# Performance work log

Hardware: AMD Instinct MI355X
Metric: run time of the kernel (lower is better)

The kernel has to match this reference:

```python
import jax, jax.numpy as jnp
import numpy as np
import math

NUM_LAYERS = 2
NUM_HEADS = 8
D_MODEL = 256
D_FF = 4 * D_MODEL
FACTOR = 5
B, L, F_IN = 8, 2048, 32


def layer_norm(x, g, b, eps=1e-5):
    m = x.mean(-1, keepdims=True)
    v = ((x - m) ** 2).mean(-1, keepdims=True)
    return (x - m) * jax.lax.rsqrt(v + eps) * g + b


def prob_attention(q, k, v, idx):
    # q,k,v: [B,H,L,Dh]; idx: [L,S] sampled key indices per query (ProbSparse)
    Bq, H, Lq, Dh = q.shape
    u = min(FACTOR * math.ceil(math.log(Lq)), Lq)  # number of 'active' queries
    k_s = k[:, :, idx, :]                              # [B,H,L,S,Dh] gathered keys
    qk_s = jnp.einsum('bhld,bhlsd->bhls', q, k_s)      # sampled scores
    M = qk_s.max(-1) - qk_s.sum(-1) / Lq               # sparsity measure [B,H,L]
    _, top = jax.lax.top_k(M, u)                       # [B,H,u] active query idx
    q_red = jnp.take_along_axis(q, top[..., None], axis=2)   # [B,H,u,Dh]
    scores = jnp.einsum('bhud,bhld->bhul', q_red, k) * (1.0 / math.sqrt(Dh))
    attn = jax.nn.softmax(scores, axis=-1)             # [B,H,u,L]
    upd = jnp.einsum('bhul,bhld->bhud', attn, v)       # [B,H,u,Dh]
    # initial context = mean of V (mask_flag=False), then scatter active rows
    ctx = jnp.broadcast_to(v.mean(2, keepdims=True), (Bq, H, Lq, Dh))
    bi = jnp.arange(Bq)[:, None, None]
    hi = jnp.arange(H)[None, :, None]
    return ctx.at[bi, hi, top].set(upd)


def setup_inputs() -> dict:
    key = jax.random.key(0)
    ks = jax.random.split(key, 16)
    S = min(FACTOR * math.ceil(math.log(L)), L)  # 40
    std = 0.02

    def w(k, shape):
        return jax.random.normal(k, shape, jnp.float32) * std

    inp = {}
    inp['x'] = jax.random.normal(ks[0], (B, L, F_IN), jnp.float32)
    inp['idx_sample'] = jax.random.randint(ks[1], (NUM_LAYERS, L, S), 0, L)
    inp['w_in'] = w(ks[2], (F_IN, D_MODEL)); inp['b_in'] = jnp.zeros((D_MODEL,), jnp.float32)
    inp['wq'] = w(ks[3], (NUM_LAYERS, D_MODEL, D_MODEL)); inp['bq'] = jnp.zeros((NUM_LAYERS, D_MODEL), jnp.float32)
    inp['wk'] = w(ks[4], (NUM_LAYERS, D_MODEL, D_MODEL)); inp['bk'] = jnp.zeros((NUM_LAYERS, D_MODEL), jnp.float32)
    inp['wv'] = w(ks[5], (NUM_LAYERS, D_MODEL, D_MODEL)); inp['bv'] = jnp.zeros((NUM_LAYERS, D_MODEL), jnp.float32)
    inp['wo'] = w(ks[6], (NUM_LAYERS, D_MODEL, D_MODEL)); inp['bo'] = jnp.zeros((NUM_LAYERS, D_MODEL), jnp.float32)
    inp['w_ff1'] = w(ks[7], (NUM_LAYERS, D_MODEL, D_FF)); inp['b_ff1'] = jnp.zeros((NUM_LAYERS, D_FF), jnp.float32)
    inp['w_ff2'] = w(ks[8], (NUM_LAYERS, D_FF, D_MODEL)); inp['b_ff2'] = jnp.zeros((NUM_LAYERS, D_MODEL), jnp.float32)
    inp['ln1_g'] = jnp.ones((NUM_LAYERS, D_MODEL), jnp.float32); inp['ln1_b'] = jnp.zeros((NUM_LAYERS, D_MODEL), jnp.float32)
    inp['ln2_g'] = jnp.ones((NUM_LAYERS, D_MODEL), jnp.float32); inp['ln2_b'] = jnp.zeros((NUM_LAYERS, D_MODEL), jnp.float32)
    inp['w_fc1'] = w(ks[9], (D_MODEL, 64)); inp['b_fc1'] = jnp.zeros((64,), jnp.float32)
    inp['w_fc2'] = w(ks[10], (64, 1)); inp['b_fc2'] = jnp.zeros((1,), jnp.float32)
    return inp


def reference(x, idx_sample, w_in, b_in, wq, bq, wk, bk, wv, bv, wo, bo,
              w_ff1, b_ff1, w_ff2, b_ff2, ln1_g, ln1_b, ln2_g, ln2_b,
              w_fc1, b_fc1, w_fc2, b_fc2):
    Bx, Lx, _ = x.shape
    h = x @ w_in + b_in  # [B,L,D_MODEL]
    for i in range(NUM_LAYERS):
        q = (h @ wq[i] + bq[i]).reshape(Bx, Lx, NUM_HEADS, -1).transpose(0, 2, 1, 3)
        k = (h @ wk[i] + bk[i]).reshape(Bx, Lx, NUM_HEADS, -1).transpose(0, 2, 1, 3)
        v = (h @ wv[i] + bv[i]).reshape(Bx, Lx, NUM_HEADS, -1).transpose(0, 2, 1, 3)
        ctx = prob_attention(q, k, v, idx_sample[i])            # [B,H,L,Dh]
        ctx = ctx.transpose(0, 2, 1, 3).reshape(Bx, Lx, D_MODEL)
        new_x = ctx @ wo[i] + bo[i]
        h = layer_norm(h + new_x, ln1_g[i], ln1_b[i])
        y = jax.nn.relu(h @ w_ff1[i] + b_ff1[i]) @ w_ff2[i] + b_ff2[i]
        h = layer_norm(h + y, ln2_g[i], ln2_b[i])
    last = h[:, -1, :]                      # take final time step
    out = jax.nn.relu(last @ w_fc1 + b_fc1) @ w_fc2 + b_fc2
    return out[:, None, :]                  # unsqueeze(1) -> [B,1,output_size]
```

## Files before the change

### kernel.cpp

```cpp
#include <hip/hip_runtime.h>
#include <math.h>

#define BB 8
#define LL 2048
#define DM 256
#define NH 8
#define DH 32
#define DFF 1024
#define SS 40
#define UU 40
#define BL (BB*LL)
#define NSL 8

#define SCP 260
#define KP  40
#define VP  34

typedef unsigned short ushort_t;
typedef unsigned char uchar_t;
typedef __attribute__((ext_vector_type(8))) short short8;
typedef __attribute__((ext_vector_type(4))) float f32x4;

__device__ inline ushort_t f2b(float f)
{
    unsigned int u = __float_as_uint(f);
    u += 0x7fff + ((u >> 16) & 1);
    return (ushort_t)(u >> 16);
}

__device__ inline float blo(unsigned int u) { return __uint_as_float(u << 16); }
__device__ inline float bhi(unsigned int u) { return __uint_as_float(u & 0xffff0000u); }

__device__ inline void gload16(const void* g, const void* l)
{
    __builtin_amdgcn_global_load_lds(
        (const __attribute__((address_space(1))) unsigned int*)g,
        (__attribute__((address_space(3))) unsigned int*)l, 16, 0, 0);
}

template<int RELU, int OUT_MODE>
__global__ __launch_bounds__(256)
void gemm_mfma(const ushort_t* __restrict__ A, const ushort_t* __restrict__ Bt,
               const float* __restrict__ bias, void* __restrict__ Cout,
               void* __restrict__ aux, int M, int N, int K)
{
    __shared__ ushort_t Asl[128 * 32];
    __shared__ ushort_t Bsl[128 * 32];

    const int t    = threadIdx.x;
    const int lane = t & 63;
    const int wv   = t >> 6;
    const int row0 = blockIdx.x * 128;
    const int col0 = blockIdx.y * 128;
    const int wr   = (wv >> 1) * 64;
    const int wc   = (wv & 1) * 64;
    const int quad = lane >> 4;
    const int l16  = lane & 15;

    f32x4 acc[4][4];
    #pragma unroll
    for (int i = 0; i < 4; ++i)
        #pragma unroll
        for (int j = 0; j < 4; ++j)
            acc[i][j] = 0.f;

    for (int k0 = 0; k0 < K; k0 += 32) {
        __syncthreads();
        #pragma unroll
        for (int r = 0; r < 2; ++r) {
            int g = r * 256 + t;
            const ushort_t* ga = A  + (size_t)(row0 + (g >> 2)) * K + k0 + (g & 3) * 8;
            const ushort_t* gb = Bt + (size_t)(col0 + (g >> 2)) * K + k0 + (g & 3) * 8;
            int lbase = (r * 256 + wv * 64) * 16;
            gload16(ga, (const char*)Asl + lbase);
            gload16(gb, (const char*)Bsl + lbase);
        }
        __syncthreads();

        short8 af[4], bfr[4];
        #pragma unroll
        for (int mi = 0; mi < 4; ++mi)
            af[mi] = *(const short8*)&Asl[(wr + mi * 16 + l16) * 32 + quad * 8];
        #pragma unroll
        for (int ni = 0; ni < 4; ++ni)
            bfr[ni] = *(const short8*)&Bsl[(wc + ni * 16 + l16) * 32 + quad * 8];
        #pragma unroll
        for (int mi = 0; mi < 4; ++mi)
            #pragma unroll
            for (int ni = 0; ni < 4; ++ni)
                acc[mi][ni] = __builtin_amdgcn_mfma_f32_16x16x32_bf16(
                    af[mi], bfr[ni], acc[mi][ni], 0, 0, 0);
    }

    #pragma unroll
    for (int mi = 0; mi < 4; ++mi) {
        #pragma unroll
        for (int ni = 0; ni < 4; ++ni) {
            int col = col0 + wc + ni * 16 + l16;
            float bb = bias[col];
            #pragma unroll
            for (int r = 0; r < 4; ++r) {
                int row = row0 + wr + mi * 16 + quad * 4 + r;
                float v = acc[mi][ni][r] + bb;
                if (RELU) v = v > 0.f ? v : 0.f;
                if (OUT_MODE == 0) {
                    ((float*)Cout)[(size_t)row * N + col] = v;
                } else if (OUT_MODE == 1) {
                    int tensor = col >> 8;
                    int c2 = col & 255;
                    int b  = row >> 11, l = row & (LL - 1);
                    int hh = c2 >> 5,  dh = c2 & 31;
                    int bh = b * NH + hh;
                    size_t bi = (((size_t)bh * LL + l) << 5) + dh;
                    ushort_t vb16 = f2b(v);
                    ((ushort_t*)Cout)[(size_t)tensor * (BB*NH*LL*DH) + bi] = vb16;
                    if (tensor == 1)
                        ((ushort_t*)aux)[(((size_t)l << 6) + bh) * 32 + dh] = vb16;
                } else if (OUT_MODE == 2) {
                    ((ushort_t*)Cout)[(size_t)row * N + col] = f2b(v);
                } else {
                    ((float*)Cout)[(size_t)row * N + col] = v;
                    ((ushort_t*)aux)[(size_t)row * N + col] = f2b(v);
                }
            }
        }
    }
}

template<int HEAD>
__global__ __launch_bounds__(256)
void gemmln_k(const ushort_t* __restrict__ A, const ushort_t* __restrict__ Bt,
              const float* __restrict__ bias, float* __restrict__ h,
              ushort_t* __restrict__ hb, const float* __restrict__ g,
              const float* __restrict__ beta, int K,
              const float* __restrict__ w1, const float* __restrict__ b1,
              const float* __restrict__ w2, const float* __restrict__ b2,
              float* __restrict__ out)
{
    __shared__ ushort_t Asl[32 * 32];
    __shared__ ushort_t Bsl[256 * 32];
    __shared__ float rs[4][32], rs2[4][32];
    __shared__ float hrowS[256];

    const int t    = threadIdx.x;
    const int lane = t & 63;
    const int wv   = t >> 6;
    const int row0 = blockIdx.x * 32;
    const int wc   = wv * 64;
    const int quad = lane >> 4;
    const int l16  = lane & 15;

    f32x4 acc[2][4];
    #pragma unroll
    for (int i = 0; i < 2; ++i)
        #pragma unroll
        for (int j = 0; j < 4; ++j)
            acc[i][j] = 0.f;

    for (int k0 = 0; k0 < K; k0 += 32) {
        __syncthreads();
        if (wv < 2) {
            const ushort_t* ga = A + (size_t)(row0 + (t >> 2)) * K + k0 + (t & 3) * 8;
            gload16(ga, (const char*)Asl + wv * 1024);
        }
        #pragma unroll
        for (int r = 0; r < 4; ++r) {
            int gg = r * 256 + t;
            const ushort_t* gb = Bt + (size_t)(gg >> 2) * K + k0 + (gg & 3) * 8;
            gload16(gb, (const char*)Bsl + (r * 256 + wv * 64) * 16);
        }
        __syncthreads();

        short8 af[2], bfr[4];
        #pragma unroll
        for (int mi = 0; mi < 2; ++mi)
            af[mi] = *(const short8*)&Asl[(mi * 16 + l16) * 32 + quad * 8];
        #pragma unroll
        for (int ni = 0; ni < 4; ++ni)
            bfr[ni] = *(const short8*)&Bsl[(wc + ni * 16 + l16) * 32 + quad * 8];
        #pragma unroll
        for (int mi = 0; mi < 2; ++mi)
            #pragma unroll
            for (int ni = 0; ni < 4; ++ni)
                acc[mi][ni] = __builtin_amdgcn_mfma_f32_16x16x32_bf16(
                    af[mi], bfr[ni], acc[mi][ni], 0, 0, 0);
    }

    float gcol[4], bcol[4];
    #pragma unroll
    for (int ni = 0; ni < 4; ++ni) {
        int col = wc + ni * 16 + l16;
        gcol[ni] = g[col];
        bcol[ni] = beta[col];
    }
    float ps[2][4], ps2[2][4];
    #pragma unroll
    for (int mi = 0; mi < 2; ++mi) {
        #pragma unroll
        for (int r = 0; r < 4; ++r) {
            int row = row0 + mi * 16 + quad * 4 + r;
            float s = 0.f, s2 = 0.f;
            #pragma unroll
            for (int ni = 0; ni < 4; ++ni) {
                int col = wc + ni * 16 + l16;
                float v = acc[mi][ni][r] + bias[col] + h[(size_t)row * DM + col];
                acc[mi][ni][r] = v;
                s += v;
                s2 += v * v;
            }
            ps[mi][r] = s;
            ps2[mi][r] = s2;
        }
    }
    #pragma unroll
    for (int off = 1; off < 16; off <<= 1) {
        #pragma unroll
        for (int mi = 0; mi < 2; ++mi)
            #pragma unroll
            for (int r = 0; r < 4; ++r) {
                ps[mi][r]  += __shfl_xor(ps[mi][r],  off, 16);
                ps2[mi][r] += __shfl_xor(ps2[mi][r], off, 16);
            }
    }
    if (l16 == 0) {
        #pragma unroll
        for (int mi = 0; mi < 2; ++mi)
            #pragma unroll
            for (int r = 0; r < 4; ++r) {
                int lrow = mi * 16 + quad * 4 + r;
                rs[wv][lrow]  = ps[mi][r];
                rs2[wv][lrow] = ps2[mi][r];
            }
    }
    __syncthreads();

    #pragma unroll
    for (int mi = 0; mi < 2; ++mi) {
        #pragma unroll
        for (int r = 0; r < 4; ++r) {
            int lrow = mi * 16 + quad * 4 + r;
            int row  = row0 + lrow;
            float tot  = rs[0][lrow] + rs[1][lrow] + rs[2][lrow] + rs[3][lrow];
            float tot2 = rs2[0][lrow] + rs2[1][lrow] + rs2[2][lrow] + rs2[3][lrow];
            float mean = tot * (1.f / (float)DM);
            float var  = tot2 * (1.f / (float)DM) - mean * mean;
            float inv  = 1.0f / sqrtf(var + 1e-5f);
            #pragma unroll
            for (int ni = 0; ni < 4; ++ni) {
                int col = wc + ni * 16 + l16;
                float val = (acc[mi][ni][r] - mean) * inv * gcol[ni] + bcol[ni];
                h[(size_t)row * DM + col]  = val;
                hb[(size_t)row * DM + col] = f2b(val);
                if (HEAD && lrow == 31) hrowS[col] = val;
            }
        }
    }

    if (HEAD) {
        __syncthreads();
        if ((blockIdx.x & 63) == 63 && t < 64) {
            int b = blockIdx.x >> 6;
            float s = 0.f;
            for (int kk = 0; kk < DM; ++kk)
                s = fmaf(hrowS[kk], w1[kk * 64 + t], s);
            s += b1[t];
            s = s > 0.f ? s : 0.f;
            float contrib = s * w2[t];
            #pragma unroll
            for (int off = 32; off > 0; off >>= 1)
                contrib += __shfl_down(contrib, off, 64);
            if (t == 0) out[b] = contrib + b2[0];
        }
    }
}

__device__ inline void tcvt_dev(float (*tile)[33], const float* __restrict__ src,
                                ushort_t* __restrict__ dst, int K, int N,
                                int matStride, int bi)
{
    int tilesN = N >> 5;
    int tpm = (K >> 5) * tilesN;
    int m   = bi / tpm;
    int tid = bi % tpm;
    int k0 = (tid / tilesN) << 5, n0 = (tid % tilesN) << 5;
    const float* s = src + (size_t)m * K * N;
    ushort_t*    d = dst + (size_t)m * matStride;
    int r = threadIdx.x >> 5, c = threadIdx.x & 31;
    #pragma unroll
    for (int i = 0; i < 4; ++i)
        tile[r + 8 * i][c] = s[(size_t)(k0 + r + 8 * i) * N + n0 + c];
    __syncthreads();
    #pragma unroll
    for (int i = 0; i < 4; ++i)
        d[(size_t)(n0 + r + 8 * i) * K + k0 + c] = f2b(tile[c][r + 8 * i]);
}

__global__ __launch_bounds__(256)
void preproc_k(const float* __restrict__ wq, const float* __restrict__ wk,
               const float* __restrict__ wv, const float* __restrict__ wo,
               const float* __restrict__ wf1, const float* __restrict__ wf2,
               const float* __restrict__ w_in,
               const float* __restrict__ bq, const float* __restrict__ bk,
               const float* __restrict__ bv, const float* __restrict__ x,
               ushort_t* __restrict__ wqkvT, ushort_t* __restrict__ woT,
               ushort_t* __restrict__ wf1T, ushort_t* __restrict__ wf2T,
               ushort_t* __restrict__ w_inT, float* __restrict__ bqkv,
               ushort_t* __restrict__ xb16)
{
    __shared__ float tile[32][33];
    int b = blockIdx.x;
    if (b < 512) {
        int which = b >> 7, lb = b & 127;
        const float* src = which == 0 ? wq : which == 1 ? wk : which == 2 ? wv : wo;
        ushort_t* dst = which == 0 ? wqkvT : which == 1 ? wqkvT + 65536
                       : which == 2 ? wqkvT + 131072 : woT;
        int stride = which == 3 ? 65536 : 768 * 256;
        tcvt_dev(tile, src, dst, DM, DM, stride, lb);
    } else if (b < 1024) {
        tcvt_dev(tile, wf1, wf1T, DM, DFF, 1024 * 256, b - 512);
    } else if (b < 1536) {
        tcvt_dev(tile, wf2, wf2T, DFF, DM, 256 * 1024, b - 1024);
    } else if (b < 1544) {
        tcvt_dev(tile, w_in, w_inT, 32, DM, 256 * 32, b - 1536);
    } else if (b < 1550) {
        int t = (b - 1544) * 256 + threadIdx.x;
        int i = t / 768, j = t % 768;
        const float* s = j < 256 ? bq : (j < 512 ? bk : bv);
        bqkv[t] = s[i * 256 + (j & 255)];
    } else {
        int tid = (b - 1550) * 256 + threadIdx.x;
        float4 v = ((const float4*)x)[tid];
        unsigned int lo = f2b(v.x) | ((unsigned int)f2b(v.y) << 16);
        unsigned int hi = f2b(v.z) | ((unsigned int)f2b(v.w) << 16);
        ((uint2*)xb16)[tid] = make_uint2(lo, hi);
    }
}

__global__ __launch_bounds__(256)
void metric2_k(const ushort_t* __restrict__ qb16, const ushort_t* __restrict__ kT,
               const int* __restrict__ idx, float* __restrict__ Mout,
               unsigned int* __restrict__ jidx32)
{
    __shared__ float mst[64][5];
    int t = threadIdx.x;
    int w = t >> 6, lane = t & 63;
    int l = blockIdx.x * 4 + w;

    if (t < 64) {
        int zb = t >> 3, sel = t & 7;
        int zl = blockIdx.x * 4 + (sel >> 1), half = sel & 1;
        jidx32[(size_t)(zb * LL + zl) * 2 + half] = 0;
    }

    float4 q[8];
    {
        const uint4* qr4 = (const uint4*)(qb16 + ((size_t)(lane * LL + l) << 5));
        #pragma unroll
        for (int i = 0; i < 4; ++i) {
            uint4 u = qr4[i];
            q[2 * i]     = make_float4(blo(u.x), bhi(u.x), blo(u.y), bhi(u.y));
            q[2 * i + 1] = make_float4(blo(u.z), bhi(u.z), blo(u.w), bhi(u.w));
        }
    }

    int r40 = idx[l * SS + (lane < SS ? lane : SS - 1)];

    float mx = -3e38f, sm = 0.f;
    for (int s = 0; s < SS; ++s) {
        int r = __shfl(r40, s, 64);
        const uint4* kr = (const uint4*)(kT + (((size_t)r << 6) + lane) * 32);
        float d = 0.f;
        #pragma unroll
        for (int ww = 0; ww < 4; ++ww) {
            uint4 kv = kr[ww];
            float4 qa = q[2 * ww], qb2 = q[2 * ww + 1];
            d = fmaf(blo(kv.x), qa.x, d);
            d = fmaf(bhi(kv.x), qa.y, d);
            d = fmaf(blo(kv.y), qa.z, d);
            d = fmaf(bhi(kv.y), qa.w, d);
            d = fmaf(blo(kv.z), qb2.x, d);
            d = fmaf(bhi(kv.z), qb2.y, d);
            d = fmaf(blo(kv.w), qb2.z, d);
            d = fmaf(bhi(kv.w), qb2.w, d);
        }
        mx = fmaxf(mx, d);
        sm += d;
    }
    mst[lane][w] = mx - sm * (1.0f / (float)LL);
    __syncthreads();

    int bh = t >> 2, ls = t & 3;
    Mout[(size_t)bh * LL + blockIdx.x * 4 + ls] = mst[bh][ls];
}

__global__ __launch_bounds__(512)
void topkf_k(const float* __restrict__ Mout, int* __restrict__ top,
             uchar_t* __restrict__ jidx)
{
    __shared__ float cvS[320];
    __shared__ int   ciS[320];
    int bh = blockIdx.x;
    int t  = threadIdx.x;
    int lane = t & 63, w = t >> 6;
    int l0 = w << 8;

    float v[4];
    #pragma unroll
    for (int i = 0; i < 4; ++i)
        v[i] = Mout[(size_t)bh * LL + l0 + i * 64 + lane];

    for (int r = 0; r < UU; ++r) {
        float bv = -3e38f; int bi = 1 << 30;
        #pragma unroll
        for (int i = 0; i < 4; ++i) {
            int idx = l0 + i * 64 + lane;
            if (v[i] > bv || (v[i] == bv && idx < bi)) { bv = v[i]; bi = idx; }
        }
        #pragma unroll
        for (int off = 32; off > 0; off >>= 1) {
            float ov = __shfl_down(bv, off, 64);
            int   oi = __shfl_down(bi, off, 64);
            if (ov > bv || (ov == bv && oi < bi)) { bv = ov; bi = oi; }
        }
        bv = __shfl(bv, 0, 64);
        bi = __shfl(bi, 0, 64);
        if (lane == 0) { cvS[w * UU + r] = bv; ciS[w * UU + r] = bi; }
        int rel = bi - l0;
        if ((rel & 63) == lane) v[rel >> 6] = -3e38f;
    }
    __syncthreads();

    for (int c = t; c < 320; c += 512) {
        float mv = cvS[c]; int mi = ciS[c];
        int rank = 0;
        for (int j = 0; j < 320; ++j)
            rank += (cvS[j] > mv) || (cvS[j] == mv && ciS[j] < mi);
        if (rank < UU) {
            top[bh * UU + rank] = mi;
            int b = bh >> 3, hh = bh & 7;
            jidx[(size_t)(b * LL + mi) * 8 + hh] = (uchar_t)(rank + 1);
        }
    }
}

__global__ __launch_bounds__(256)
void attnupd_k(const ushort_t* __restrict__ qb16, const ushort_t* __restrict__ kb16,
               const ushort_t* __restrict__ vb16, const int* __restrict__ top,
               float* __restrict__ mP, float* __restrict__ sP,
               float* __restrict__ OP, float* __restrict__ vmeanP)
{
    __shared__ ushort_t qs[48 * KP];
    __shared__ ushort_t kv[256 * KP];
    __shared__ float    sc[48 * SCP];
    __shared__ float    msh[UU];
    __shared__ float    red[8][32];

    int blk = blockIdx.x;
    int sl  = blk & (NSL - 1);
    int bh  = blk >> 3;
    int t   = threadIdx.x;
    int l0  = sl << 8;
    int lane = t & 63, wvx = t >> 6;
    int quad = lane >> 4, l16 = lane & 15;
    const float scale = 0.17677669529663687f;

    for (int i = t; i < 48 * 32; i += 256) {
        int j = i >> 5, dd = i & 31;
        qs[(i >> 5) * KP + dd] = (j < UU)
            ? qb16[((size_t)(bh * LL + top[bh * UU + j]) << 5) + dd] : (ushort_t)0;
    }
    {
        const unsigned int* krow =
            (const unsigned int*)(kb16 + ((size_t)(bh * LL + l0 + t) << 5));
        #pragma unroll
        for (int i = 0; i < 16; ++i)
            ((unsigned int*)kv)[t * (KP / 2) + i] = krow[i];
    }
    __syncthreads();

    {
        short8 afq[3];
        #pragma unroll
        for (int mt = 0; mt < 3; ++mt)
            afq[mt] = *(const short8*)&qs[(mt * 16 + l16) * KP + quad * 8];
        #pragma unroll
        for (int n4 = 0; n4 < 4; ++n4) {
            int nt = wvx * 4 + n4;
            short8 bk = *(const short8*)&kv[(nt * 16 + l16) * KP + quad * 8];
            #pragma unroll
            for (int mt = 0; mt < 3; ++mt) {
                f32x4 dd = {0.f, 0.f, 0.f, 0.f};
                dd = __builtin_amdgcn_mfma_f32_16x16x32_bf16(afq[mt], bk, dd, 0, 0, 0);
                #pragma unroll
                for (int r = 0; r < 4; ++r)
                    sc[(mt * 16 + quad * 4 + r) * SCP + nt * 16 + l16] = dd[r] * scale;
            }
        }
    }
    __syncthreads();

    int j8 = t >> 5, d = t & 31;
    #pragma unroll
    for (int g = 0; g < 5; ++g) {
        int j = g * 8 + j8;
        float4 a = *(const float4*)&sc[j * SCP + 4 * d];
        float4 b = *(const float4*)&sc[j * SCP + 128 + 4 * d];
        float m = fmaxf(fmaxf(fmaxf(a.x, a.y), fmaxf(a.z, a.w)),
                        fmaxf(fmaxf(b.x, b.y), fmaxf(b.z, b.w)));
        #pragma unroll
        for (int off = 16; off > 0; off >>= 1)
            m = fmaxf(m, __shfl_down(m, off, 64));
        if (d == 0) msh[j] = m;
    }
    __syncthreads();

    #pragma unroll 2
    for (int i = t; i < UU * 64; i += 256) {
        int j = i >> 6;
        float* p = &sc[j * SCP + (i & 63) * 4];
        float4 e = *(float4*)p;
        float mm = msh[j];
        e.x = __expf(e.x - mm); e.y = __expf(e.y - mm);
        e.z = __expf(e.z - mm); e.w = __expf(e.w - mm);
        *(float4*)p = e;
    }
    __syncthreads();

    int pq = bh * NSL + sl;

    #pragma unroll
    for (int g = 0; g < 5; ++g) {
        int j = g * 8 + j8;
        float4 a = *(const float4*)&sc[j * SCP + 4 * d];
        float4 b = *(const float4*)&sc[j * SCP + 128 + 4 * d];
        float s = a.x + a.y + a.z + a.w + b.x + b.y + b.z + b.w;
        #pragma unroll
        for (int off = 16; off > 0; off >>= 1)
            s += __shfl_down(s, off, 64);
        if (d == 0) { sP[pq * UU + j] = s; mP[pq * UU + j] = msh[j]; }
    }
    {
        const unsigned int* vrow =
            (const unsigned int*)(vb16 + ((size_t)(bh * LL + l0 + t) << 5));
        #pragma unroll
        for (int i = 0; i < 16; ++i)
            *(unsigned int*)&kv[t * VP + 2 * i] = vrow[i];
        const ushort_t* base = vb16 + ((size_t)(bh * LL + l0 + j8 * 32) << 5) + d;
        float s = 0.f;
        #pragma unroll 8
        for (int i = 0; i < 32; ++i)
            s += __uint_as_float((unsigned int)base[(size_t)i << 5] << 16);
        red[j8][d] = s;
    }
    __syncthreads();

    if (t < 32) {
        float tot = 0.f;
        #pragma unroll
        for (int p = 0; p < 8; ++p) tot += red[p][t];
        vmeanP[pq * 32 + t] = tot;
    }

    if (wvx < 3) {
        f32x4 acc0 = {0.f, 0.f, 0.f, 0.f};
        f32x4 acc1 = {0.f, 0.f, 0.f, 0.f};
        #pragma unroll
        for (int ks = 0; ks < 8; ++ks) {
            float4 p0 = *(const float4*)&sc[(wvx * 16 + l16) * SCP + ks * 32 + quad * 8];
            float4 p1 = *(const float4*)&sc[(wvx * 16 + l16) * SCP + ks * 32 + quad * 8 + 4];
            short8 af;
            af[0] = (short)f2b(p0.x); af[1] = (short)f2b(p0.y);
            af[2] = (short)f2b(p0.z); af[3] = (short)f2b(p0.w);
            af[4] = (short)f2b(p1.x); af[5] = (short)f2b(p1.y);
            af[6] = (short)f2b(p1.z); af[7] = (short)f2b(p1.w);
            #pragma unroll
            for (int nt = 0; nt < 2; ++nt) {
                short8 bf;
                #pragma unroll
                for (int jj = 0; jj < 8; ++jj)
                    bf[jj] = (short)kv[(ks * 32 + quad * 8 + jj) * VP + nt * 16 + l16];
                if (nt == 0)
                    acc0 = __builtin_amdgcn_mfma_f32_16x16x32_bf16(af, bf, acc0, 0, 0, 0);
                else
                    acc1 = __builtin_amdgcn_mfma_f32_16x16x32_bf16(af, bf, acc1, 0, 0, 0);
            }
        }
        #pragma unroll
        for (int r = 0; r < 4; ++r) {
            int j = wvx * 16 + quad * 4 + r;
            if (j < UU) {
                OP[((size_t)pq * UU + j) * 32 + l16]      = acc0[r];
                OP[((size_t)pq * UU + j) * 32 + 16 + l16] = acc1[r];
            }
        }
    }
}

__global__ __launch_bounds__(256)
void fillcomb_k(const float* __restrict__ vmeanP, const uchar_t* __restrict__ jidx,
                const float* __restrict__ mP, const float* __restrict__ sP,
                const float* __restrict__ OP, ushort_t* __restrict__ ctxb)
{
    int tid = blockIdx.x * 256 + threadIdx.x;
    int pr   = tid & 127;
    int rowi = tid >> 7;
    int b    = rowi >> 11;
    int hh   = pr >> 4;
    int bh   = b * 8 + hh;
    int d0   = (pr * 2) & 31;
    int j    = (int)jidx[(size_t)rowi * 8 + hh];

    float v0, v1;
    if (j == 0) {
        float s0 = 0.f, s1 = 0.f;
        #pragma unroll
        for (int q = 0; q < NSL; ++q) {
            s0 += vmeanP[(bh * NSL + q) * 32 + d0];
            s1 += vmeanP[(bh * NSL + q) * 32 + d0 + 1];
        }
        v0 = s0 * (1.f / (float)LL);
        v1 = s1 * (1.f / (float)LL);
    } else {
        int jj = j - 1;
        float M = -3e38f;
        #pragma unroll
        for (int q = 0; q < NSL; ++q) M = fmaxf(M, mP[(bh * NSL + q) * UU + jj]);
        float S = 0.f, O0 = 0.f, O1 = 0.f;
        #pragma unroll
        for (int q = 0; q < NSL; ++q) {
            float wgt = __expf(mP[(bh * NSL + q) * UU + jj] - M);
            S  = fmaf(sP[(bh * NSL + q) * UU + jj], wgt, S);
            O0 = fmaf(OP[((size_t)(bh * NSL + q) * UU + jj) * 32 + d0], wgt, O0);
            O1 = fmaf(OP[((size_t)(bh * NSL + q) * UU + jj) * 32 + d0 + 1], wgt, O1);
        }
        v0 = O0 / S;
        v1 = O1 / S;
    }
    ((unsigned int*)ctxb)[tid] = (unsigned int)f2b(v0) | ((unsigned int)f2b(v1) << 16);
}

extern "C" void kernel_launch(void* const* d_in, const int* in_sizes, int n_in,
                              void* d_out, int out_size, void* d_ws, size_t ws_size,
                              hipStream_t stream)
{
    const float* x    = (const float*)d_in[0];
    const int*   idx  = (const int*)  d_in[1];
    const float* w_in = (const float*)d_in[2];
    const float* b_in = (const float*)d_in[3];
    const float* wq   = (const float*)d_in[4];
    const float* bq   = (const float*)d_in[5];
    const float* wk   = (const float*)d_in[6];
    const float* bk   = (const float*)d_in[7];
    const float* wv   = (const float*)d_in[8];
    const float* bv   = (const float*)d_in[9];
    const float* wo   = (const float*)d_in[10];
    const float* bo   = (const float*)d_in[11];
    const float* wf1  = (const float*)d_in[12];
    const float* bf1  = (const float*)d_in[13];
    const float* wf2  = (const float*)d_in[14];
    const float* bf2  = (const float*)d_in[15];
    const float* g1   = (const float*)d_in[16];
    const float* be1  = (const float*)d_in[17];
    const float* g2   = (const float*)d_in[18];
    const float* be2  = (const float*)d_in[19];
    const float* wfc1 = (const float*)d_in[20];
    const float* bfc1 = (const float*)d_in[21];
    const float* wfc2 = (const float*)d_in[22];
    const float* bfc2 = (const float*)d_in[23];
    float* out = (float*)d_out;

    float* ws = (float*)d_ws;
    float*    h     = ws;
    ushort_t* q16   = (ushort_t*)(ws + 4194304);
    ushort_t* k16   = q16 + 4194304;
    ushort_t* v16   = q16 + 8388608;
    ushort_t* ctxb  = q16;
    ushort_t* ffbb  = (ushort_t*)(ws + 6291456);
    float*    attnS = ws + 16777216;
    ushort_t* kT16  = (ushort_t*)attnS;
    float*    Mbuf  = attnS + 2097152;
    float*    vmeP  = attnS + 2269184;
    float*    OP    = attnS + 2285568;
    float*    mP    = attnS + 2940928;
    float*    sP    = attnS + 2961408;
    uchar_t*  jidx  = (uchar_t*)(attnS + 2981888);
    float*    scr   = ws + 20971520;
    ushort_t* xb16  = (ushort_t*)scr;
    int*      top   = (int*)(scr + 264192);
    ushort_t* hb    = (ushort_t*)(scr + 266752);
    ushort_t* wqkvT = (ushort_t*)(scr + 2363904);
    ushort_t* woT   = (ushort_t*)(scr + 2560512);
    ushort_t* wf1T  = (ushort_t*)(scr + 2626048);
    ushort_t* wf2T  = (ushort_t*)(scr + 2888192);
    ushort_t* w_inT = (ushort_t*)(scr + 3150336);
    float*    bqkv  = scr + 3154432;

    dim3 blk(256);

    preproc_k<<<dim3(2062), blk, 0, stream>>>(
        wq, wk, wv, wo, wf1, wf2, w_in, bq, bk, bv, x,
        wqkvT, woT, wf1T, wf2T, w_inT, bqkv, xb16);

    gemm_mfma<0,3><<<dim3(BL/128, 2), blk, 0, stream>>>(
        xb16, w_inT, b_in, (void*)h, (void*)hb, BL, DM, 32);

    for (int i = 0; i < 2; ++i) {
        gemm_mfma<0,1><<<dim3(BL/128, 6), blk, 0, stream>>>(
            hb, wqkvT + (size_t)i*768*256, bqkv + i*768, (void*)q16, (void*)kT16,
            BL, 768, DM);

        metric2_k<<<dim3(512), blk, 0, stream>>>(
            q16, kT16, idx + (size_t)i*LL*SS, Mbuf, (unsigned int*)jidx);
        topkf_k<<<dim3(BB*NH), dim3(512), 0, stream>>>(Mbuf, top, jidx);
        attnupd_k<<<dim3(BB*NH*NSL), blk, 0, stream>>>(q16, k16, v16, top, mP, sP, OP, vmeP);
        fillcomb_k<<<dim3(BL*DM/512), blk, 0, stream>>>(vmeP, jidx, mP, sP, OP, ctxb);

        gemmln_k<0><<<dim3(BL/32), blk, 0, stream>>>(
            ctxb, woT + (size_t)i*256*256, bo + i*DM, h, hb,
            g1 + i*DM, be1 + i*DM, DM,
            nullptr, nullptr, nullptr, nullptr, nullptr);

        gemm_mfma<1,2><<<dim3(BL/128, 8), blk, 0, stream>>>(
            hb, wf1T + (size_t)i*1024*256, bf1 + i*DFF, (void*)ffbb, nullptr, BL, DFF, DM);

        if (i == 1) {
            gemmln_k<1><<<dim3(BL/32), blk, 0, stream>>>(
                ffbb, wf2T + (size_t)i*256*1024, bf2 + i*DM, h, hb,
                g2 + i*DM, be2 + i*DM, DFF,
                wfc1, bfc1, wfc2, bfc2, out);
        } else {
            gemmln_k<0><<<dim3(BL/32), blk, 0, stream>>>(
                ffbb, wf2T + (size_t)i*256*1024, bf2 + i*DM, h, hb,
                g2 + i*DM, be2 + i*DM, DFF,
                nullptr, nullptr, nullptr, nullptr, nullptr);
        }
    }
}
```

Measured before the change: 464.3 us.

## Split fused GEMM+LayerNorm into tiled MFMA GEMM plus separate add-LayerNorm kernel

Replaces the fused gemmln kernel, whose 32-row tiles reload the full 256-column weight slice for every block, with the general 128-row tiled gemm_mfma writing an fp32 intermediate. A new lightweight addln kernel then does the residual add and LayerNorm per row, one wavefront per row, with the final MLP head in the last block per batch. This aims to get better weight reuse and MFMA efficiency in the GEMM. In exchange it adds an extra launch and a round trip of an fp32 [BL,256] buffer through global memory.

Result: slower. 490.7 us (+5.7%).

```diff
diff --git a/kernel.cpp b/kernel.cpp
--- a/kernel.cpp
+++ b/kernel.cpp
@@ -129,147 +129,64 @@
 
 template<int HEAD>
 __global__ __launch_bounds__(256)
-void gemmln_k(const ushort_t* __restrict__ A, const ushort_t* __restrict__ Bt,
-              const float* __restrict__ bias, float* __restrict__ h,
-              ushort_t* __restrict__ hb, const float* __restrict__ g,
-              const float* __restrict__ beta, int K,
-              const float* __restrict__ w1, const float* __restrict__ b1,
-              const float* __restrict__ w2, const float* __restrict__ b2,
-              float* __restrict__ out)
-{
-    __shared__ ushort_t Asl[32 * 32];
-    __shared__ ushort_t Bsl[256 * 32];
-    __shared__ float rs[4][32], rs2[4][32];
+void addln_k(float* __restrict__ h, ushort_t* __restrict__ hb,
+             const float* __restrict__ nx,
+             const float* __restrict__ g, const float* __restrict__ beta,
+             const float* __restrict__ w1, const float* __restrict__ b1,
+             const float* __restrict__ w2, const float* __restrict__ b2,
+             float* __restrict__ out)
+{
     __shared__ float hrowS[256];
-
-    const int t    = threadIdx.x;
-    const int lane = t & 63;
-    const int wv   = t >> 6;
-    const int row0 = blockIdx.x * 32;
-    const int wc   = wv * 64;
-    const int quad = lane >> 4;
-    const int l16  = lane & 15;
-
-    f32x4 acc[2][4];
-    #pragma unroll
-    for (int i = 0; i < 2; ++i)
-        #pragma unroll
-        for (int j = 0; j < 4; ++j)
-            acc[i][j] = 0.f;
-
-    for (int k0 = 0; k0 < K; k0 += 32) {
+    int lane = threadIdx.x & 63;
+    int wv   = threadIdx.x >> 6;
+    int row  = blockIdx.x * 4 + wv;
+    size_t i4 = (size_t)row * 64 + lane;
+    float4 a = ((const float4*)h)[i4];
+    float4 b = ((const float4*)nx)[i4];
+    float4 xv = make_float4(a.x + b.x, a.y + b.y, a.z + b.z, a.w + b.w);
+    float s  = xv.x + xv.y + xv.z + xv.w;
+    float s2 = xv.x * xv.x + xv.y * xv.y + xv.z * xv.z + xv.w * xv.w;
+    #pragma unroll
+    for (int off = 32; off > 0; off >>= 1) {
+        s  += __shfl_down(s, off, 64);
+        s2 += __shfl_down(s2, off, 64);
+    }
+    float m   = __shfl(s, 0, 64) * (1.f / (float)DM);
+    float var = __shfl(s2, 0, 64) * (1.f / (float)DM) - m * m;
+    float inv = 1.0f / sqrtf(var + 1e-5f);
+    float4 gg = ((const float4*)g)[lane];
+    float4 be = ((const float4*)beta)[lane];
+    float4 r;
+    r.x = (xv.x - m) * inv * gg.x + be.x;
+    r.y = (xv.y - m) * inv * gg.y + be.y;
+    r.z = (xv.z - m) * inv * gg.z + be.z;
+    r.w = (xv.w - m) * inv * gg.w + be.w;
+    ((float4*)h)[i4] = r;
+    unsigned int lo = f2b(r.x) | ((unsigned int)f2b(r.y) << 16);
+    unsigned int hi = f2b(r.z) | ((unsigned int)f2b(r.w) << 16);
+    ((uint2*)hb)[i4] = make_uint2(lo, hi);
+
+    if (HEAD) {
+        bool headblk = ((blockIdx.x & 511) == 511);
+        if (headblk && wv == 3) {
+            hrowS[lane * 4 + 0] = r.x;
+            hrowS[lane * 4 + 1] = r.y;
+            hrowS[lane * 4 + 2] = r.z;
+            hrowS[lane * 4 + 3] = r.w;
+        }
         __syncthreads();
-        if (wv < 2) {
-            const ushort_t* ga = A + (size_t)(row0 + (t >> 2)) * K + k0 + (t & 3) * 8;
-            gload16(ga, (const char*)Asl + wv * 1024);
-        }
-        #pragma unroll
-        for (int r = 0; r < 4; ++r) {
-            int gg = r * 256 + t;
-            const ushort_t* gb = Bt + (size_t)(gg >> 2) * K + k0 + (gg & 3) * 8;
-            gload16(gb, (const char*)Bsl + (r * 256 + wv * 64) * 16);
-        }
-        __syncthreads();
-
-        short8 af[2], bfr[4];
-        #pragma unroll
-        for (int mi = 0; mi < 2; ++mi)
-            af[mi] = *(const short8*)&Asl[(mi * 16 + l16) * 32 + quad * 8];
-        #pragma unroll
-        for (int ni = 0; ni < 4; ++ni)
-            bfr[ni] = *(const short8*)&Bsl[(wc + ni * 16 + l16) * 32 + quad * 8];
-        #pragma unroll
-        for (int mi = 0; mi < 2; ++mi)
-            #pragma unroll
-            for (int ni = 0; ni < 4; ++ni)
-                acc[mi][ni] = __builtin_amdgcn_mfma_f32_16x16x32_bf16(
-                    af[mi], bfr[ni], acc[mi][ni], 0, 0, 0);
-    }
-
-    float gcol[4], bcol[4];
-    #pragma unroll
-    for (int ni = 0; ni < 4; ++ni) {
-        int col = wc + ni * 16 + l16;
-        gcol[ni] = g[col];
-        bcol[ni] = beta[col];
-    }
-    float ps[2][4], ps2[2][4];
-    #pragma unroll
-    for (int mi = 0; mi < 2; ++mi) {
-        #pragma unroll
-        for (int r = 0; r < 4; ++r) {
-            int row = row0 + mi * 16 + quad * 4 + r;
-            float s = 0.f, s2 = 0.f;
-            #pragma unroll
-            for (int ni = 0; ni < 4; ++ni) {
-                int col = wc + ni * 16 + l16;
-                float v = acc[mi][ni][r] + bias[col] + h[(size_t)row * DM + col];
-                acc[mi][ni][r] = v;
-                s += v;
-                s2 += v * v;
-            }
-            ps[mi][r] = s;
-            ps2[mi][r] = s2;
-        }
-    }
-    #pragma unroll
-    for (int off = 1; off < 16; off <<= 1) {
-        #pragma unroll
-        for (int mi = 0; mi < 2; ++mi)
-            #pragma unroll
-            for (int r = 0; r < 4; ++r) {
-                ps[mi][r]  += __shfl_xor(ps[mi][r],  off, 16);
-                ps2[mi][r] += __shfl_xor(ps2[mi][r], off, 16);
-            }
-    }
-    if (l16 == 0) {
-        #pragma unroll
-        for (int mi = 0; mi < 2; ++mi)
-            #pragma unroll
-            for (int r = 0; r < 4; ++r) {
-                int lrow = mi * 16 + quad * 4 + r;
-                rs[wv][lrow]  = ps[mi][r];
-                rs2[wv][lrow] = ps2[mi][r];
-            }
-    }
-    __syncthreads();
-
-    #pragma unroll
-    for (int mi = 0; mi < 2; ++mi) {
-        #pragma unroll
-        for (int r = 0; r < 4; ++r) {
-            int lrow = mi * 16 + quad * 4 + r;
-            int row  = row0 + lrow;
-            float tot  = rs[0][lrow] + rs[1][lrow] + rs[2][lrow] + rs[3][lrow];
-            float tot2 = rs2[0][lrow] + rs2[1][lrow] + rs2[2][lrow] + rs2[3][lrow];
-            float mean = tot * (1.f / (float)DM);
-            float var  = tot2 * (1.f / (float)DM) - mean * mean;
-            float inv  = 1.0f / sqrtf(var + 1e-5f);
-            #pragma unroll
-            for (int ni = 0; ni < 4; ++ni) {
-                int col = wc + ni * 16 + l16;
-                float val = (acc[mi][ni][r] - mean) * inv * gcol[ni] + bcol[ni];
-                h[(size_t)row * DM + col]  = val;
-                hb[(size_t)row * DM + col] = f2b(val);
-                if (HEAD && lrow == 31) hrowS[col] = val;
-            }
-        }
-    }
-
-    if (HEAD) {
-        __syncthreads();
-        if ((blockIdx.x & 63) == 63 && t < 64) {
-            int b = blockIdx.x >> 6;
-            float s = 0.f;
+        if (headblk && threadIdx.x < 64) {
+            int j = threadIdx.x;
+            float sh = 0.f;
             for (int kk = 0; kk < DM; ++kk)
-                s = fmaf(hrowS[kk], w1[kk * 64 + t], s);
-            s += b1[t];
-            s = s > 0.f ? s : 0.f;
-            float contrib = s * w2[t];
+                sh = fmaf(hrowS[kk], w1[kk * 64 + j], sh);
+            sh += b1[j];
+            sh = sh > 0.f ? sh : 0.f;
+            float contrib = sh * w2[j];
             #pragma unroll
             for (int off = 32; off > 0; off >>= 1)
                 contrib += __shfl_down(contrib, off, 64);
-            if (t == 0) out[b] = contrib + b2[0];
+            if (j == 0) out[blockIdx.x >> 9] = contrib + b2[0];
         }
     }
 }
@@ -684,6 +601,7 @@
     float*    mP    = attnS + 2940928;
     float*    sP    = attnS + 2961408;
     uchar_t*  jidx  = (uchar_t*)(attnS + 2981888);
+    float*    newx  = attnS;
     float*    scr   = ws + 20971520;
     ushort_t* xb16  = (ushort_t*)scr;
     int*      top   = (int*)(scr + 264192);
@@ -715,23 +633,24 @@
         attnupd_k<<<dim3(BB*NH*NSL), blk, 0, stream>>>(q16, k16, v16, top, mP, sP, OP, vmeP);
         fillcomb_k<<<dim3(BL*DM/512), blk, 0, stream>>>(vmeP, jidx, mP, sP, OP, ctxb);
 
-        gemmln_k<0><<<dim3(BL/32), blk, 0, stream>>>(
-            ctxb, woT + (size_t)i*256*256, bo + i*DM, h, hb,
-            g1 + i*DM, be1 + i*DM, DM,
+        gemm_mfma<0,0><<<dim3(BL/128, 2), blk, 0, stream>>>(
+            ctxb, woT + (size_t)i*256*256, bo + i*DM, (void*)newx, nullptr, BL, DM, DM);
+        addln_k<0><<<dim3(BL/4), blk, 0, stream>>>(
+            h, hb, newx, g1 + i*DM, be1 + i*DM,
             nullptr, nullptr, nullptr, nullptr, nullptr);
 
         gemm_mfma<1,2><<<dim3(BL/128, 8), blk, 0, stream>>>(
             hb, wf1T + (size_t)i*1024*256, bf1 + i*DFF, (void*)ffbb, nullptr, BL, DFF, DM);
 
+        gemm_mfma<0,0><<<dim3(BL/128, 2), blk, 0, stream>>>(
+            ffbb, wf2T + (size_t)i*256*1024, bf2 + i*DM, (void*)newx, nullptr, BL, DM, DFF);
         if (i == 1) {
-            gemmln_k<1><<<dim3(BL/32), blk, 0, stream>>>(
-                ffbb, wf2T + (size_t)i*256*1024, bf2 + i*DM, h, hb,
-                g2 + i*DM, be2 + i*DM, DFF,
+            addln_k<1><<<dim3(BL/4), blk, 0, stream>>>(
+                h, hb, newx, g2 + i*DM, be2 + i*DM,
                 wfc1, bfc1, wfc2, bfc2, out);
         } else {
-            gemmln_k<0><<<dim3(BL/32), blk, 0, stream>>>(
-                ffbb, wf2T + (size_t)i*256*1024, bf2 + i*DM, h, hb,
-                g2 + i*DM, be2 + i*DM, DFF,
+            addln_k<0><<<dim3(BL/4), blk, 0, stream>>>(
+                h, hb, newx, g2 + i*DM, be2 + i*DM,
                 nullptr, nullptr, nullptr, nullptr, nullptr);
         }
     }
```

## Split top-k into parallel rank-based candidate pass and merge pass

Applied to the files above, without the earlier changes.

Replaces the single-block-per-head iterative top-40 selection (40 sequential wave argmax rounds) with two kernels. The first runs 256 blocks, each wave ranking 128 values by counting comparisons in shared memory and keeping its top 40 candidates. The second merges the 640 candidates per head by rank counting. This spreads the selection over more blocks and removes the serial argmax loop, at the cost of an extra launch and a global round-trip for the candidates.

Result: no change. 470.8 us (+1.4%).

```diff
diff --git a/kernel.cpp b/kernel.cpp
--- a/kernel.cpp
+++ b/kernel.cpp
@@ -393,48 +393,53 @@
     Mout[(size_t)bh * LL + blockIdx.x * 4 + ls] = mst[bh][ls];
 }
 
+__global__ __launch_bounds__(256)
+void topk1r_k(const float* __restrict__ Mout,
+              float* __restrict__ cand_v, int* __restrict__ cand_i)
+{
+    __shared__ float sl[4][128];
+    int blk = blockIdx.x;
+    int bh  = blk >> 2, sg = blk & 3;
+    int t   = threadIdx.x;
+    int w   = t >> 6, lane = t & 63;
+    int slice = sg * 4 + w;
+    int l0    = slice * 128;
+    const float* src = Mout + (size_t)bh * LL + l0;
+
+    float v0 = src[lane];
+    float v1 = src[lane + 64];
+    sl[w][lane]      = v0;
+    sl[w][lane + 64] = v1;
+
+    int r0 = 0, r1 = 0;
+    #pragma unroll 8
+    for (int i = 0; i < 128; ++i) {
+        float ov = sl[w][i];
+        r0 += (ov > v0) || (ov == v0 && i < lane);
+        r1 += (ov > v1) || (ov == v1 && i < lane + 64);
+    }
+    int base = (bh * 16 + slice) * UU;
+    if (r0 < UU) { cand_v[base + r0] = v0; cand_i[base + r0] = l0 + lane; }
+    if (r1 < UU) { cand_v[base + r1] = v1; cand_i[base + r1] = l0 + lane + 64; }
+}
+
 __global__ __launch_bounds__(512)
-void topkf_k(const float* __restrict__ Mout, int* __restrict__ top,
-             uchar_t* __restrict__ jidx)
-{
-    __shared__ float cvS[320];
-    __shared__ int   ciS[320];
-    int bh = blockIdx.x;
-    int t  = threadIdx.x;
-    int lane = t & 63, w = t >> 6;
-    int l0 = w << 8;
-
-    float v[4];
-    #pragma unroll
-    for (int i = 0; i < 4; ++i)
-        v[i] = Mout[(size_t)bh * LL + l0 + i * 64 + lane];
-
-    for (int r = 0; r < UU; ++r) {
-        float bv = -3e38f; int bi = 1 << 30;
-        #pragma unroll
-        for (int i = 0; i < 4; ++i) {
-            int idx = l0 + i * 64 + lane;
-            if (v[i] > bv || (v[i] == bv && idx < bi)) { bv = v[i]; bi = idx; }
-        }
-        #pragma unroll
-        for (int off = 32; off > 0; off >>= 1) {
-            float ov = __shfl_down(bv, off, 64);
-            int   oi = __shfl_down(bi, off, 64);
-            if (ov > bv || (ov == bv && oi < bi)) { bv = ov; bi = oi; }
-        }
-        bv = __shfl(bv, 0, 64);
-        bi = __shfl(bi, 0, 64);
-        if (lane == 0) { cvS[w * UU + r] = bv; ciS[w * UU + r] = bi; }
-        int rel = bi - l0;
-        if ((rel & 63) == lane) v[rel >> 6] = -3e38f;
-    }
-    __syncthreads();
-
-    for (int c = t; c < 320; c += 512) {
-        float mv = cvS[c]; int mi = ciS[c];
+void topk2r_k(const float* __restrict__ cand_v, const int* __restrict__ cand_i,
+              int* __restrict__ top, uchar_t* __restrict__ jidx)
+{
+    __shared__ float cv[640];
+    __shared__ int   ci[640];
+    int bh = blockIdx.x, t = threadIdx.x;
+    for (int i = t; i < 640; i += 512) {
+        cv[i] = cand_v[bh * 640 + i];
+        ci[i] = cand_i[bh * 640 + i];
+    }
+    __syncthreads();
+    for (int c = t; c < 640; c += 512) {
+        float mv = cv[c]; int mi = ci[c];
         int rank = 0;
-        for (int j = 0; j < 320; ++j)
-            rank += (cvS[j] > mv) || (cvS[j] == mv && ciS[j] < mi);
+        for (int j = 0; j < 640; ++j)
+            rank += (cv[j] > mv) || (cv[j] == mv && ci[j] < mi);
         if (rank < UU) {
             top[bh * UU + rank] = mi;
             int b = bh >> 3, hh = bh & 7;
@@ -679,11 +684,13 @@
     float*    attnS = ws + 16777216;
     ushort_t* kT16  = (ushort_t*)attnS;
     float*    Mbuf  = attnS + 2097152;
+    float*    candv = attnS + 2228224;
     float*    vmeP  = attnS + 2269184;
     float*    OP    = attnS + 2285568;
     float*    mP    = attnS + 2940928;
     float*    sP    = attnS + 2961408;
     uchar_t*  jidx  = (uchar_t*)(attnS + 2981888);
+    int*      candi = (int*)(attnS + 3014656);
     float*    scr   = ws + 20971520;
     ushort_t* xb16  = (ushort_t*)scr;
     int*      top   = (int*)(scr + 264192);
@@ -711,7 +718,8 @@
 
         metric2_k<<<dim3(512), blk, 0, stream>>>(
             q16, kT16, idx + (size_t)i*LL*SS, Mbuf, (unsigned int*)jidx);
-        topkf_k<<<dim3(BB*NH), dim3(512), 0, stream>>>(Mbuf, top, jidx);
+        topk1r_k<<<dim3(256), blk, 0, stream>>>(Mbuf, candv, candi);
+        topk2r_k<<<dim3(BB*NH), dim3(512), 0, stream>>>(candv, candi, top, jidx);
         attnupd_k<<<dim3(BB*NH*NSL), blk, 0, stream>>>(q16, k16, v16, top, mP, sP, OP, vmeP);
         fillcomb_k<<<dim3(BL*DM/512), blk, 0, stream>>>(vmeP, jidx, mP, sP, OP, ctxb);
 
```
